# Performance work log

Measured on AMD Instinct MI355X. Metric: run time of the kernel, lower is better.

The kernel has to match this reference:

```python
import jax, jax.numpy as jnp
import numpy as np

MRG = 0.1
ALPHA = 32.0
STAT_WEIGHT = 0.01
STAT_ADJUST_WEIGHT = 0.15
COS_EPS = 1e-8  # torch F.cosine_similarity eps


def l2_norm(x):
    # matches torch l2_norm: x / sqrt(sum(x^2, axis=1) + 1e-12)
    normp = jnp.sum(x * x, axis=1) + 1e-12
    return x / jnp.sqrt(normp)[:, None]


def setup_inputs() -> dict:
    key = jax.random.key(0)
    kx, kt, kp, kc = jax.random.split(key, 4)
    B, C, D = 512, 50000, 128
    X = jax.random.normal(kx, (B, D), dtype=jnp.float32)
    T = jax.random.randint(kt, (B,), 0, C, dtype=jnp.int32)
    proxies = jax.random.normal(kp, (C, D), dtype=jnp.float32)
    class_centers = jax.random.normal(kc, (C, D), dtype=jnp.float32)
    return {"X": X, "T": T, "proxies": proxies, "class_centers": class_centers}


def reference(X, T, proxies, class_centers):
    C = proxies.shape[0]
    Xn = l2_norm(X)                      # (B, D)
    Pn = l2_norm(proxies)                # (C, D)
    cos = Xn @ Pn.T                      # (B, C)

    # ---- vectorized per-class statistics (replaces the Python loop) ----
    counts = jax.ops.segment_sum(jnp.ones(T.shape[0], jnp.float32), T, num_segments=C)
    sums = jax.ops.segment_sum(Xn, T, num_segments=C)          # (C, D)
    sqs = jax.ops.segment_sum(Xn * Xn, T, num_segments=C)      # (C, D)
    safe = jnp.maximum(counts, 1.0)[:, None]
    mean = sums / safe
    var = jnp.clip(sqs / safe - mean * mean, 1e-6, 10.0)        # biased var, clamped
    var_weight = 1.0 / (1.0 + var.mean(axis=1))                 # (C,)

    # cosine_similarity(P_norm[i], class_centers[i]) with torch eps semantics
    pnorm = jnp.maximum(jnp.sqrt(jnp.sum(Pn * Pn, axis=1)), COS_EPS)
    cnorm = jnp.maximum(jnp.sqrt(jnp.sum(class_centers * class_centers, axis=1)), COS_EPS)
    center_sim = jnp.sum(Pn * class_centers, axis=1) / (pnorm * cnorm)  # (C,)

    has_samples = counts > 0
    adj = jnp.where(has_samples, center_sim * var_weight * STAT_ADJUST_WEIGHT, 0.0)
    combined = cos + adj[None, :]        # (B, C)

    # ---- proxy-anchor exp-sum terms ----
    onehot = (T[:, None] == jnp.arange(C, dtype=T.dtype)[None, :])  # (B, C) bool
    pos_exp = jnp.exp(-ALPHA * (combined - MRG))
    neg_exp = jnp.exp(ALPHA * (combined + MRG))
    P_sim_sum = jnp.sum(jnp.where(onehot, pos_exp, 0.0), axis=0)    # (C,)
    N_sim_sum = jnp.sum(jnp.where(onehot, 0.0, neg_exp), axis=0)    # (C,)

    num_valid = jnp.sum(has_samples).astype(jnp.float32)
    pos_term = jnp.sum(jnp.log1p(P_sim_sum)) / num_valid
    neg_term = jnp.sum(jnp.log1p(N_sim_sum)) / jnp.float32(C)

    center_reg = jnp.mean(jnp.abs(class_centers))
    return pos_term + neg_term + STAT_WEIGHT * center_reg
```

## Files before the change

### kernel.cpp

```cpp
#include <hip/hip_runtime.h>
#include <math.h>

#define ALPHA 32.0f
#define MRG 0.1f
#define STAT_WEIGHT 0.01f
#define STAT_ADJ_W 0.15f
#define COS_EPS 1e-8f

typedef __attribute__((ext_vector_type(8))) short bf16x8;
typedef __attribute__((ext_vector_type(4))) float f32x4;
typedef __attribute__((ext_vector_type(4))) unsigned int u32x4;

__device__ __forceinline__ ushort f2bf(float f) {
    unsigned u = __float_as_uint(f);
    return (ushort)((u + 0x7FFFu + ((u >> 16) & 1u)) >> 16);
}
__device__ __forceinline__ unsigned pk2(float a, float b) {
    return (unsigned)f2bf(a) | ((unsigned)f2bf(b) << 16);
}

__device__ __forceinline__ float bredL(float v, float* sm, int tid) {
    #pragma unroll
    for (int off = 1; off < 64; off <<= 1) v += __shfl_xor(v, off);
    if ((tid & 63) == 0 && tid < 128) sm[tid >> 6] = v;
    __syncthreads();
    float r = sm[0] + sm[1];
    __syncthreads();
    return r;
}

__launch_bounds__(256, 2)
__global__ void k_ms(const float* __restrict__ X, const float* __restrict__ proxies,
                     const float* __restrict__ cc, const int* __restrict__ T,
                     float* __restrict__ PN, float* __restrict__ adj,
                     float* __restrict__ cabs_part, float* __restrict__ scal,
                     int C, int B, int nslice) {
    const int tid = threadIdx.x, lane = tid & 63, wv = tid >> 6;
    const int nlo = lane & 15, quad = lane >> 4;
    const int bid = blockIdx.x;
    const int x = bid & 255, half = bid >> 8;

    __shared__ ushort Sx[32768];
    __shared__ alignas(16) int Tg[256];
    __shared__ float sm[2];
    __shared__ float smc[4];
    __shared__ int mcnt;

    if (bid == 0 && tid < 8) scal[tid] = 0.f;

    {
        const int row = tid;
        const float4* xr = (const float4*)(X + (size_t)(half * 256 + row) * 128);
        float s32[32];
        #pragma unroll
        for (int g = 0; g < 32; ++g) {
            float4 v = xr[g];
            s32[g] = (v.x * v.x + v.y * v.y) + (v.z * v.z + v.w * v.w);
        }
        #pragma unroll
        for (int w = 16; w >= 1; w >>= 1)
            #pragma unroll
            for (int g = 0; g < w; ++g) s32[g] = s32[2 * g] + s32[2 * g + 1];
        float pin = rsqrtf(s32[0] + 1e-12f);
        uint4* dst = (uint4*)Sx + row * 16;
        #pragma unroll
        for (int g = 0; g < 16; ++g) {
            float4 a = xr[g * 2], b4 = xr[g * 2 + 1];
            u32x4 u;
            u.x = pk2(a.x * pin, a.y * pin);
            u.y = pk2(a.z * pin, a.w * pin);
            u.z = pk2(b4.x * pin, b4.y * pin);
            u.w = pk2(b4.z * pin, b4.w * pin);
            dst[g ^ (row & 15)] = __builtin_bit_cast(uint4, u);
        }
    }
    Tg[tid] = T[half * 256 + tid];
    __syncthreads();

    float* PA = PN + (size_t)half * 2 * C;
    float* NA = PA + C;

    int fro[4];
    #pragma unroll
    for (int ks = 0; ks < 4; ++ks)
        fro[ks] = nlo * 128 + (((ks * 4 + quad) ^ nlo) << 3);

    const int s0 = (x + (half ? 128 : 0)) & 255;
    for (int s = s0; s < nslice; s += 256) {
        const int c0 = s * 128;
        const int cls0 = c0 + wv * 32 + nlo;
        const int cls1 = cls0 + 16;

        bf16x8 bfr[2][4];
        #pragma unroll
        for (int t = 0; t < 2; ++t) {
            int cls = c0 + wv * 32 + t * 16 + nlo;
            int cl = (cls < C) ? cls : C - 1;
            const float4* pr = (const float4*)(proxies + (size_t)cl * 128);
            float4 v0[4], v1[4];
            float s2 = 0.f;
            #pragma unroll
            for (int ks = 0; ks < 4; ++ks) {
                v0[ks] = pr[ks * 8 + quad * 2];
                v1[ks] = pr[ks * 8 + quad * 2 + 1];
                s2 += v0[ks].x*v0[ks].x + v0[ks].y*v0[ks].y + v0[ks].z*v0[ks].z + v0[ks].w*v0[ks].w
                    + v1[ks].x*v1[ks].x + v1[ks].y*v1[ks].y + v1[ks].z*v1[ks].z + v1[ks].w*v1[ks].w;
            }
            s2 += __shfl_xor(s2, 16);
            s2 += __shfl_xor(s2, 32);
            float pin = rsqrtf(s2 + 1e-12f);
            #pragma unroll
            for (int ks = 0; ks < 4; ++ks) {
                u32x4 u;
                u.x = pk2(v0[ks].x * pin, v0[ks].y * pin);
                u.y = pk2(v0[ks].z * pin, v0[ks].w * pin);
                u.z = pk2(v1[ks].x * pin, v1[ks].y * pin);
                u.w = pk2(v1[ks].z * pin, v1[ks].w * pin);
                bfr[t][ks] = __builtin_bit_cast(bf16x8, u);
            }
        }

        float pp0 = 0.f, np0 = 0.f, pp1 = 0.f, np1 = 0.f;
        #pragma unroll 4
        for (int rt = 0; rt < 16; ++rt) {
            const ushort* sb = &Sx[rt * 2048];
            bf16x8 a0 = *(const bf16x8*)&sb[fro[0]];
            bf16x8 a1 = *(const bf16x8*)&sb[fro[1]];
            bf16x8 a2 = *(const bf16x8*)&sb[fro[2]];
            bf16x8 a3 = *(const bf16x8*)&sb[fro[3]];
            f32x4 acc0 = {0.f,0.f,0.f,0.f}, acc1 = {0.f,0.f,0.f,0.f};
            acc0 = __builtin_amdgcn_mfma_f32_16x16x32_bf16(a0, bfr[0][0], acc0, 0, 0, 0);
            acc1 = __builtin_amdgcn_mfma_f32_16x16x32_bf16(a0, bfr[1][0], acc1, 0, 0, 0);
            acc0 = __builtin_amdgcn_mfma_f32_16x16x32_bf16(a1, bfr[0][1], acc0, 0, 0, 0);
            acc1 = __builtin_amdgcn_mfma_f32_16x16x32_bf16(a1, bfr[1][1], acc1, 0, 0, 0);
            acc0 = __builtin_amdgcn_mfma_f32_16x16x32_bf16(a2, bfr[0][2], acc0, 0, 0, 0);
            acc1 = __builtin_amdgcn_mfma_f32_16x16x32_bf16(a2, bfr[1][2], acc1, 0, 0, 0);
            acc0 = __builtin_amdgcn_mfma_f32_16x16x32_bf16(a3, bfr[0][3], acc0, 0, 0, 0);
            acc1 = __builtin_amdgcn_mfma_f32_16x16x32_bf16(a3, bfr[1][3], acc1, 0, 0, 0);

            int4 t4 = *(const int4*)&Tg[rt * 16 + quad * 4];
            int tvs[4] = {t4.x, t4.y, t4.z, t4.w};
            #pragma unroll
            for (int r = 0; r < 4; ++r) {
                { bool po = (tvs[r] == cls0); float v = acc0[r];
                  float e = __expf(po ? -ALPHA * (v - MRG) : ALPHA * (v + MRG));
                  pp0 += po ? e : 0.f; np0 += po ? 0.f : e; }
                { bool po = (tvs[r] == cls1); float v = acc1[r];
                  float e = __expf(po ? -ALPHA * (v - MRG) : ALPHA * (v + MRG));
                  pp1 += po ? e : 0.f; np1 += po ? 0.f : e; }
            }
        }

        pp0 += __shfl_xor(pp0, 16); pp0 += __shfl_xor(pp0, 32);
        np0 += __shfl_xor(np0, 16); np0 += __shfl_xor(np0, 32);
        pp1 += __shfl_xor(pp1, 16); pp1 += __shfl_xor(pp1, 32);
        np1 += __shfl_xor(np1, 16); np1 += __shfl_xor(np1, 32);
        if (quad == 0) {
            if (cls0 < C) { PA[cls0] = pp0; NA[cls0] = np0; }
            if (cls1 < C) { PA[cls1] = pp1; NA[cls1] = np1; }
        }
    }

    __syncthreads();
    int* Tl = (int*)Sx;
    int* mlist = (int*)Sx + 512;
    const int b = bid;
    const int d = tid & 127;
    const bool lo = tid < 128;

    Tl[tid] = T[tid]; Tl[tid + 256] = T[tid + 256];
    if (tid == 0) mcnt = 0;

    float cabs = 0.f;
    {
        const float4* cp = (const float4*)cc;
        const int n4 = C * 32;
        #pragma unroll 4
        for (int i = b * 256 + tid; i < n4; i += B * 256) {
            float4 v = cp[i];
            cabs += fabsf(v.x) + fabsf(v.y) + fabsf(v.z) + fabsf(v.w);
        }
    }
    #pragma unroll
    for (int off = 1; off < 64; off <<= 1) cabs += __shfl_xor(cabs, off);
    if (lane == 0) smc[wv] = cabs;
    __syncthreads();
    if (tid == 0) cabs_part[b] = (smc[0] + smc[1]) + (smc[2] + smc[3]);

    const int c = Tl[b];

    for (int j = tid; j < B; j += 256)
        if (Tl[j] == c) mlist[atomicAdd(&mcnt, 1)] = j;
    __syncthreads();
    const int cnt = mcnt;
    int minj = mlist[0];
    for (int i = 1; i < cnt; ++i) minj = min(minj, mlist[i]);
    if (minj != b) return;

    float sd = 0.f, qd = 0.f;
    int prev = -1;
    for (int rank = 0; rank < cnt; ++rank) {
        int cur = 0x7fffffff;
        for (int i = 0; i < cnt; ++i) { int v = mlist[i]; if (v > prev && v < cur) cur = v; }
        prev = cur;
        float xj = lo ? X[(size_t)cur * 128 + d] : 0.f;
        float nj = bredL(xj * xj, sm, tid);
        float xnj = xj * rsqrtf(nj + 1e-12f);
        sd += xnj; qd += xnj * xnj;
    }
    float fc = (float)cnt;
    float m = sd / fc;
    float var = fminf(fmaxf(qd / fc - m * m, 1e-6f), 10.0f);
    float sv = bredL(var, sm, tid);

    float p  = lo ? proxies[(size_t)c * 128 + d] : 0.f;
    float cv = lo ? cc[(size_t)c * 128 + d] : 0.f;
    float s2 = bredL(p * p, sm, tid);
    float c2 = bredL(cv * cv, sm, tid);
    float pc = bredL(p * cv, sm, tid);
    if (tid == 0) {
        float inv = rsqrtf(s2 + 1e-12f);
        float pn = fmaxf(sqrtf(s2) * inv, COS_EPS);
        float cn = fmaxf(sqrtf(c2), COS_EPS);
        float censim = (pc * inv) / (pn * cn);
        float vw = 1.0f / (1.0f + sv * (1.0f / 128.0f));
        adj[c] = censim * vw * STAT_ADJ_W;
    }
}

__launch_bounds__(256)
__global__ void k_fin(const float* __restrict__ PN, const float* __restrict__ adj,
                      const float* __restrict__ cabs_part, float* __restrict__ scal,
                      float* __restrict__ out, int C, int nfin) {
    const int tid = threadIdx.x, lane = tid & 63, wv = tid >> 6;
    const int c = blockIdx.x * 256 + tid;
    __shared__ float red[4][3];
    float lp = 0.f, ln = 0.f, nv = 0.f;
    if (c < C) {
        float p = PN[c] + PN[2 * (size_t)C + c];
        float n = PN[(size_t)C + c] + PN[3 * (size_t)C + c];
        float a = 0.f;
        if (p > 0.f) { a = adj[c]; nv = 1.f; }
        lp = log1pf(p * __expf(-ALPHA * a));
        ln = log1pf(n * __expf( ALPHA * a));
    }
    #pragma unroll
    for (int off = 1; off < 64; off <<= 1) {
        lp += __shfl_xor(lp, off);
        ln += __shfl_xor(ln, off);
        nv += __shfl_xor(nv, off);
    }
    if (lane == 0) { red[wv][0] = lp; red[wv][1] = ln; red[wv][2] = nv; }
    __syncthreads();
    if (tid == 0) {
        atomicAdd(&scal[0], red[0][0] + red[1][0] + red[2][0] + red[3][0]);
        atomicAdd(&scal[1], red[0][1] + red[1][1] + red[2][1] + red[3][1]);
        atomicAdd(&scal[3], red[0][2] + red[1][2] + red[2][2] + red[3][2]);
    }
    if (blockIdx.x == 0) {
        float cb = cabs_part[tid] + cabs_part[tid + 256];
        #pragma unroll
        for (int off = 1; off < 64; off <<= 1) cb += __shfl_xor(cb, off);
        __syncthreads();
        if (lane == 0) red[wv][0] = cb;
        __syncthreads();
        if (tid == 0) atomicAdd(&scal[2], red[0][0] + red[1][0] + red[2][0] + red[3][0]);
    }
    if (tid == 0) {
        __threadfence();
        unsigned old = atomicAdd((unsigned*)(scal + 4), 1u);
        if (old == (unsigned)(nfin - 1)) {
            float S0 = atomicAdd(&scal[0], 0.f);
            float S1 = atomicAdd(&scal[1], 0.f);
            float S2 = atomicAdd(&scal[2], 0.f);
            float S3 = atomicAdd(&scal[3], 0.f);
            out[0] = S0 / S3 + S1 / (float)C + STAT_WEIGHT * (S2 / ((float)C * 128.f));
        }
    }
}

extern "C" void kernel_launch(void* const* d_in, const int* in_sizes, int n_in,
                              void* d_out, int out_size, void* d_ws, size_t ws_size,
                              hipStream_t stream) {
    const float* X       = (const float*)d_in[0];
    const int*   T       = (const int*)d_in[1];
    const float* proxies = (const float*)d_in[2];
    const float* cc      = (const float*)d_in[3];
    float* out = (float*)d_out;

    const int B = in_sizes[1];
    const int D = in_sizes[0] / B;
    const int C = in_sizes[2] / D;

    float*  PN   = (float*)d_ws;
    float*  scal = PN + 4 * (size_t)C;
    float*  cabs_part = scal + 8;
    float*  adj  = cabs_part + 512;

    const int nslice = (C + 127) / 128;
    const int nfin   = (C + 255) / 256;

    k_ms<<<B, 256, 0, stream>>>(X, proxies, cc, T, PN, adj, cabs_part,
                                scal, C, B, nslice);
    k_fin<<<nfin, 256, 0, stream>>>(PN, adj, cabs_part, scal, out, C, nfin);
}
```

Baseline: 136.6 us.

## Move class stats and final reduction into a second kernel, merging finalize

The per-class statistics and center-abs reduction move out of the main GEMM/exp kernel into a second kernel that also does the final log1p reduction, so k_fin is gone. The main kernel loses its tail work and shared-memory extras, which may improve its occupancy and keep it from stalling on the serial per-class loop. The second kernel handles present classes per owner block and uses a strided loop for classes with no samples. The center-abs sum now goes straight to a global atomic instead of a partial array.

```diff
diff --git a/kernel.cpp b/kernel.cpp
--- a/kernel.cpp
+++ b/kernel.cpp
@@ -30,11 +30,9 @@
 }
 
 __launch_bounds__(256, 2)
-__global__ void k_ms(const float* __restrict__ X, const float* __restrict__ proxies,
-                     const float* __restrict__ cc, const int* __restrict__ T,
-                     float* __restrict__ PN, float* __restrict__ adj,
-                     float* __restrict__ cabs_part, float* __restrict__ scal,
-                     int C, int B, int nslice) {
+__global__ void k_main(const float* __restrict__ X, const float* __restrict__ proxies,
+                       const int* __restrict__ T, float* __restrict__ PN,
+                       float* __restrict__ scal, int C, int nslice) {
     const int tid = threadIdx.x, lane = tid & 63, wv = tid >> 6;
     const int nlo = lane & 15, quad = lane >> 4;
     const int bid = blockIdx.x;
@@ -42,9 +40,6 @@
 
     __shared__ ushort Sx[32768];
     __shared__ alignas(16) int Tg[256];
-    __shared__ float sm[2];
-    __shared__ float smc[4];
-    __shared__ int mcnt;
 
     if (bid == 0 && tid < 8) scal[tid] = 0.f;
 
@@ -160,13 +155,22 @@
             if (cls1 < C) { PA[cls1] = pp1; NA[cls1] = np1; }
         }
     }
-
-    __syncthreads();
-    int* Tl = (int*)Sx;
-    int* mlist = (int*)Sx + 512;
-    const int b = bid;
+}
+
+__global__ void k_sf(const float* __restrict__ X, const float* __restrict__ proxies,
+                     const float* __restrict__ cc, const int* __restrict__ T,
+                     const float* __restrict__ PN, float* __restrict__ scal,
+                     float* __restrict__ out, int C, int B, int nblk) {
+    const int tid = threadIdx.x, b = blockIdx.x;
+    const int lane = tid & 63, wv = tid >> 6;
     const int d = tid & 127;
     const bool lo = tid < 128;
+    __shared__ int Tl[512];
+    __shared__ int mlist[512];
+    __shared__ float sm[2];
+    __shared__ float smc[4];
+    __shared__ float red[4][3];
+    __shared__ int mcnt;
 
     Tl[tid] = T[tid]; Tl[tid + 256] = T[tid + 256];
     if (tid == 0) mcnt = 0;
@@ -176,7 +180,7 @@
         const float4* cp = (const float4*)cc;
         const int n4 = C * 32;
         #pragma unroll 4
-        for (int i = b * 256 + tid; i < n4; i += B * 256) {
+        for (int i = b * 256 + tid; i < n4; i += nblk * 256) {
             float4 v = cp[i];
             cabs += fabsf(v.x) + fabsf(v.y) + fabsf(v.z) + fabsf(v.w);
         }
@@ -185,7 +189,7 @@
     for (int off = 1; off < 64; off <<= 1) cabs += __shfl_xor(cabs, off);
     if (lane == 0) smc[wv] = cabs;
     __syncthreads();
-    if (tid == 0) cabs_part[b] = (smc[0] + smc[1]) + (smc[2] + smc[3]);
+    if (tid == 0) atomicAdd(&scal[2], (smc[0] + smc[1]) + (smc[2] + smc[3]));
 
     const int c = Tl[b];
 
@@ -195,55 +199,52 @@
     const int cnt = mcnt;
     int minj = mlist[0];
     for (int i = 1; i < cnt; ++i) minj = min(minj, mlist[i]);
-    if (minj != b) return;
-
-    float sd = 0.f, qd = 0.f;
-    int prev = -1;
-    for (int rank = 0; rank < cnt; ++rank) {
-        int cur = 0x7fffffff;
-        for (int i = 0; i < cnt; ++i) { int v = mlist[i]; if (v > prev && v < cur) cur = v; }
-        prev = cur;
-        float xj = lo ? X[(size_t)cur * 128 + d] : 0.f;
-        float nj = bredL(xj * xj, sm, tid);
-        float xnj = xj * rsqrtf(nj + 1e-12f);
-        sd += xnj; qd += xnj * xnj;
-    }
-    float fc = (float)cnt;
-    float m = sd / fc;
-    float var = fminf(fmaxf(qd / fc - m * m, 1e-6f), 10.0f);
-    float sv = bredL(var, sm, tid);
-
-    float p  = lo ? proxies[(size_t)c * 128 + d] : 0.f;
-    float cv = lo ? cc[(size_t)c * 128 + d] : 0.f;
-    float s2 = bredL(p * p, sm, tid);
-    float c2 = bredL(cv * cv, sm, tid);
-    float pc = bredL(p * cv, sm, tid);
-    if (tid == 0) {
-        float inv = rsqrtf(s2 + 1e-12f);
-        float pn = fmaxf(sqrtf(s2) * inv, COS_EPS);
-        float cn = fmaxf(sqrtf(c2), COS_EPS);
-        float censim = (pc * inv) / (pn * cn);
-        float vw = 1.0f / (1.0f + sv * (1.0f / 128.0f));
-        adj[c] = censim * vw * STAT_ADJ_W;
-    }
-}
-
-__launch_bounds__(256)
-__global__ void k_fin(const float* __restrict__ PN, const float* __restrict__ adj,
-                      const float* __restrict__ cabs_part, float* __restrict__ scal,
-                      float* __restrict__ out, int C, int nfin) {
-    const int tid = threadIdx.x, lane = tid & 63, wv = tid >> 6;
-    const int c = blockIdx.x * 256 + tid;
-    __shared__ float red[4][3];
+
     float lp = 0.f, ln = 0.f, nv = 0.f;
-    if (c < C) {
-        float p = PN[c] + PN[2 * (size_t)C + c];
-        float n = PN[(size_t)C + c] + PN[3 * (size_t)C + c];
-        float a = 0.f;
-        if (p > 0.f) { a = adj[c]; nv = 1.f; }
-        lp = log1pf(p * __expf(-ALPHA * a));
-        ln = log1pf(n * __expf( ALPHA * a));
-    }
+
+    if (minj == b) {
+        float sd = 0.f, qd = 0.f;
+        int prev = -1;
+        for (int rank = 0; rank < cnt; ++rank) {
+            int cur = 0x7fffffff;
+            for (int i = 0; i < cnt; ++i) { int v = mlist[i]; if (v > prev && v < cur) cur = v; }
+            prev = cur;
+            float xj = lo ? X[(size_t)cur * 128 + d] : 0.f;
+            float nj = bredL(xj * xj, sm, tid);
+            float xnj = xj * rsqrtf(nj + 1e-12f);
+            sd += xnj; qd += xnj * xnj;
+        }
+        float fc = (float)cnt;
+        float m = sd / fc;
+        float var = fminf(fmaxf(qd / fc - m * m, 1e-6f), 10.0f);
+        float sv = bredL(var, sm, tid);
+
+        float p  = lo ? proxies[(size_t)c * 128 + d] : 0.f;
+        float cv = lo ? cc[(size_t)c * 128 + d] : 0.f;
+        float s2 = bredL(p * p, sm, tid);
+        float c2 = bredL(cv * cv, sm, tid);
+        float pc = bredL(p * cv, sm, tid);
+        if (tid == 0) {
+            float inv = rsqrtf(s2 + 1e-12f);
+            float pn = fmaxf(sqrtf(s2) * inv, COS_EPS);
+            float cn = fmaxf(sqrtf(c2), COS_EPS);
+            float censim = (pc * inv) / (pn * cn);
+            float vw = 1.0f / (1.0f + sv * (1.0f / 128.0f));
+            float a = censim * vw * STAT_ADJ_W;
+            float pt = PN[c] + PN[2 * (size_t)C + c];
+            float nt = PN[(size_t)C + c] + PN[3 * (size_t)C + c];
+            lp = log1pf(pt * __expf(-ALPHA * a));
+            ln = log1pf(nt * __expf( ALPHA * a));
+            nv = 1.f;
+        }
+    }
+
+    for (int cl = b * 256 + tid; cl < C; cl += nblk * 256) {
+        float pt = PN[cl] + PN[2 * (size_t)C + cl];
+        if (!(pt > 0.f))
+            ln += log1pf(PN[(size_t)C + cl] + PN[3 * (size_t)C + cl]);
+    }
+
     #pragma unroll
     for (int off = 1; off < 64; off <<= 1) {
         lp += __shfl_xor(lp, off);
@@ -256,20 +257,9 @@
         atomicAdd(&scal[0], red[0][0] + red[1][0] + red[2][0] + red[3][0]);
         atomicAdd(&scal[1], red[0][1] + red[1][1] + red[2][1] + red[3][1]);
         atomicAdd(&scal[3], red[0][2] + red[1][2] + red[2][2] + red[3][2]);
-    }
-    if (blockIdx.x == 0) {
-        float cb = cabs_part[tid] + cabs_part[tid + 256];
-        #pragma unroll
-        for (int off = 1; off < 64; off <<= 1) cb += __shfl_xor(cb, off);
-        __syncthreads();
-        if (lane == 0) red[wv][0] = cb;
-        __syncthreads();
-        if (tid == 0) atomicAdd(&scal[2], red[0][0] + red[1][0] + red[2][0] + red[3][0]);
-    }
-    if (tid == 0) {
         __threadfence();
         unsigned old = atomicAdd((unsigned*)(scal + 4), 1u);
-        if (old == (unsigned)(nfin - 1)) {
+        if (old == (unsigned)(nblk - 1)) {
             float S0 = atomicAdd(&scal[0], 0.f);
             float S1 = atomicAdd(&scal[1], 0.f);
             float S2 = atomicAdd(&scal[2], 0.f);
@@ -292,15 +282,11 @@
     const int D = in_sizes[0] / B;
     const int C = in_sizes[2] / D;
 
-    float*  PN   = (float*)d_ws;
-    float*  scal = PN + 4 * (size_t)C;
-    float*  cabs_part = scal + 8;
-    float*  adj  = cabs_part + 512;
+    float* PN   = (float*)d_ws;
+    float* scal = PN + 4 * (size_t)C;
 
     const int nslice = (C + 127) / 128;
-    const int nfin   = (C + 255) / 256;
-
-    k_ms<<<B, 256, 0, stream>>>(X, proxies, cc, T, PN, adj, cabs_part,
-                                scal, C, B, nslice);
-    k_fin<<<nfin, 256, 0, stream>>>(PN, adj, cabs_part, scal, out, C, nfin);
-}
+
+    k_main<<<512, 256, 0, stream>>>(X, proxies, T, PN, scal, C, nslice);
+    k_sf<<<B, 256, 0, stream>>>(X, proxies, cc, T, PN, scal, out, C, B, B);
+}
```

Result: slower. 155.4 us (+13.7%).
